# Performance work log

Hardware: AMD Instinct MI355X
Metric: run time of the kernel (lower is better)

The kernel has to match this reference:

```python
import jax, jax.numpy as jnp
import numpy as np

N = 100_000      # nodes
E = 800_000      # edges per edge type
T = 3            # num_edge_types - 1 relation-specific convs
D_IN = 128
D_OUT = 128


def setup_inputs() -> dict:
    key = jax.random.key(0)
    k1, k2, k3, k4 = jax.random.split(key, 4)
    x = jax.random.normal(k1, (N, D_IN), dtype=jnp.float32)
    edges = jax.random.randint(k2, (T, 2, E), 0, N, dtype=jnp.int32)
    W = jax.random.normal(k3, (T, D_IN, D_OUT), dtype=jnp.float32) * (1.0 / np.sqrt(D_IN))
    b = jax.random.normal(k4, (T, D_OUT), dtype=jnp.float32) * 0.02
    return {"x": x, "edges": edges, "W": W, "b": b}


def _gcn_conv(x, ei, W, b):
    """PyG GCNConv: add self-loops, symmetric D^-1/2 (A+I) D^-1/2 norm, XW, +b."""
    n = x.shape[0]
    xw = x @ W                                   # [N, D_OUT]
    loop = jnp.arange(n, dtype=ei.dtype)
    src = jnp.concatenate([ei[0], loop])         # [E+N]
    dst = jnp.concatenate([ei[1], loop])         # [E+N]
    deg = jax.ops.segment_sum(jnp.ones(src.shape[0], xw.dtype), dst, num_segments=n)
    dis = jnp.where(deg > 0, jax.lax.rsqrt(jnp.maximum(deg, 1e-12)), 0.0)
    norm = dis[src] * dis[dst]                   # [E+N]
    msg = xw[src] * norm[:, None]                # gather-transform: [E+N, D_OUT]
    out = jax.ops.segment_sum(msg, dst, num_segments=n)  # scatter-add back to nodes
    return out + b


def reference(x, edges, W, b):
    # Sum of per-edge-type GCN convolutions into a shared output buffer.
    out = jnp.zeros((x.shape[0], W.shape[-1]), dtype=x.dtype)
    for i in range(edges.shape[0]):              # small fixed relation loop
        out = out + _gcn_conv(x, edges[i], W[i], b[i])
    return out
```

## Files before the change

### kernel.cpp

```cpp
#include <hip/hip_runtime.h>

#define NN 100000
#define EE 800000
#define TT 3
#define D  128
#define NB 391
#define CAPB 7168
#define CHUNK 8192
#define LSTRIDE 392
#define ENC 32767.0f

typedef unsigned short bf16_t;

typedef __bf16 bf16x8_t __attribute__((ext_vector_type(8)));
typedef float  f32x4_t  __attribute__((ext_vector_type(4)));

union ABFrag { bf16x8_t v; uint4 q; };

__device__ __forceinline__ bf16_t f2bf(float f) {
    unsigned u = __float_as_uint(f);
    u += 0x7fff + ((u >> 16) & 1);
    return (bf16_t)(u >> 16);
}
__device__ __forceinline__ float bf_lo(unsigned p) { return __uint_as_float(p << 16); }
__device__ __forceinline__ float bf_hi(unsigned p) { return __uint_as_float(p & 0xFFFF0000u); }

__global__ void quant_kernel(const float* __restrict__ x, bf16_t* __restrict__ xq) {
    int i = (blockIdx.x * 256 + threadIdx.x) * 4;
    if (i >= NN * D) return;
    float4 f = *(const float4*)(x + i);
    uint2 p;
    p.x = (unsigned)f2bf(f.x) | ((unsigned)f2bf(f.y) << 16);
    p.y = (unsigned)f2bf(f.z) | ((unsigned)f2bf(f.w) << 16);
    *(uint2*)(xq + i) = p;
}

__global__ void wconv_kernel(const float* __restrict__ W, bf16_t* __restrict__ WT) {
    int t = blockIdx.y, n = blockIdx.x, k = threadIdx.x;
    WT[((size_t)t * D + n) * D + k] = f2bf(W[((size_t)t * D + k) * D + n]);
}

__global__ __launch_bounds__(512, 4) void bin_kernel(const int* __restrict__ edges,
                                                     int* __restrict__ bcnt,
                                                     unsigned* __restrict__ bin) {
    __shared__ int hist[NB];
    __shared__ int lbase[NB];
    __shared__ int gbase[NB];
    __shared__ int scn[512];
    __shared__ unsigned srec[CHUNK];
    __shared__ unsigned stgt[CHUNK];
    int tid = threadIdx.x;
    int t = blockIdx.y;
    int f0 = blockIdx.x * CHUNK;
    const int* sb = edges + (size_t)t * 2 * EE;
    const int* db = sb + EE;

    for (int i = tid; i < NB; i += 512) hist[i] = 0;
    __syncthreads();

    int4 s4[4], d4[4];
    int rnk[16];
    bool have[4];
#pragma unroll
    for (int j = 0; j < 4; ++j) {
        int e = f0 + ((j * 512 + tid) << 2);
        have[j] = (e < EE);
        if (have[j]) { s4[j] = *(const int4*)(sb + e); d4[j] = *(const int4*)(db + e); }
    }
#pragma unroll
    for (int j = 0; j < 4; ++j) {
        if (have[j]) {
            rnk[j * 4 + 0] = atomicAdd(&hist[d4[j].x >> 8], 1);
            rnk[j * 4 + 1] = atomicAdd(&hist[d4[j].y >> 8], 1);
            rnk[j * 4 + 2] = atomicAdd(&hist[d4[j].z >> 8], 1);
            rnk[j * 4 + 3] = atomicAdd(&hist[d4[j].w >> 8], 1);
        }
    }
    __syncthreads();

    int hv = (tid < NB) ? hist[tid] : 0;
    scn[tid] = hv;
    __syncthreads();
    for (int off = 1; off < 512; off <<= 1) {
        int u = 0;
        if (tid >= off) u = scn[tid - off];
        __syncthreads();
        if (tid >= off) scn[tid] += u;
        __syncthreads();
    }
    if (tid < NB) {
        lbase[tid] = scn[tid] - hv;
        gbase[tid] = (hv > 0) ? atomicAdd(&bcnt[tid], hv) : 0;
    }
    __syncthreads();

#pragma unroll
    for (int j = 0; j < 4; ++j) {
        if (have[j]) {
            int ss[4] = {s4[j].x, s4[j].y, s4[j].z, s4[j].w};
            int dd[4] = {d4[j].x, d4[j].y, d4[j].z, d4[j].w};
#pragma unroll
            for (int k = 0; k < 4; ++k) {
                int bkt = dd[k] >> 8;
                int r = rnk[j * 4 + k];
                int pos = lbase[bkt] + r;
                int rel = gbase[bkt] + r;
                srec[pos] = ((unsigned)(dd[k] & 255) << 19) | ((unsigned)t << 17) | (unsigned)ss[k];
                stgt[pos] = (rel < CAPB) ? (unsigned)(bkt * CAPB + rel) : 0xFFFFFFFFu;
            }
        }
    }
    __syncthreads();

    int nval = EE - f0; if (nval > CHUNK) nval = CHUNK;
    for (int i = tid; i < nval; i += 512) {
        unsigned tg = stgt[i];
        if (tg != 0xFFFFFFFFu) bin[tg] = srec[i];
    }
}

#define MAXR 14
__global__ __launch_bounds__(512) void sort_kernel(const int* __restrict__ bcnt,
                                                   unsigned* __restrict__ bin,
                                                   float* __restrict__ dis3,
                                                   int* __restrict__ cnts3,
                                                   int* __restrict__ nodeoff) {
    __shared__ int cnt[768];
    __shared__ int tot[256];
    int tid = threadIdx.x;
    int b = blockIdx.x;
    int c = bcnt[b]; if (c > CAPB) c = CAPB;
    unsigned* reg = bin + (size_t)b * CAPB;

    for (int i = tid; i < 768; i += 512) cnt[i] = 0;
    __syncthreads();

    unsigned ur[MAXR];
    int rr[MAXR];
    bool vld[MAXR];
#pragma unroll
    for (int k = 0; k < MAXR; ++k) {
        int i = tid + k * 512;
        vld[k] = (i < c);
        unsigned u = vld[k] ? reg[i] : 0u;
        ur[k] = u;
        int bi = (int)(u >> 19) * 3 + (int)((u >> 17) & 3);
        rr[k] = vld[k] ? atomicAdd(&cnt[bi], 1) : 0;
    }
    __syncthreads();

    int d0 = 0, d1 = 0, d2 = 0;
    if (tid < 256) {
        d0 = cnt[tid * 3]; d1 = cnt[tid * 3 + 1]; d2 = cnt[tid * 3 + 2];
        tot[tid] = d0 + d1 + d2;
    }
    __syncthreads();
    for (int off = 1; off < 256; off <<= 1) {
        int v = 0;
        if (tid < 256 && tid >= off) v = tot[tid - off];
        __syncthreads();
        if (tid < 256 && tid >= off) tot[tid] += v;
        __syncthreads();
    }
    if (tid < 256) {
        int excl = tot[tid] - (d0 + d1 + d2);
        int gnode = b * 256 + tid;
        if (gnode < NN) {
            nodeoff[gnode] = b * CAPB + excl;
            cnts3[gnode]   = d0 | (d1 << 8) | (d2 << 16);
            dis3[gnode]            = rsqrtf((float)d0 + 1.f);
            dis3[NN + gnode]       = rsqrtf((float)d1 + 1.f);
            dis3[2 * NN + gnode]   = rsqrtf((float)d2 + 1.f);
        }
        cnt[tid * 3]     = excl;
        cnt[tid * 3 + 1] = excl + d0;
        cnt[tid * 3 + 2] = excl + d0 + d1;
    }
    __syncthreads();
#pragma unroll
    for (int k = 0; k < MAXR; ++k) {
        if (vld[k]) {
            unsigned u = ur[k];
            int bi = (int)(u >> 19) * 3 + (int)((u >> 17) & 3);
            reg[cnt[bi] + rr[k]] = u & 0x7FFFFu;
        }
    }
}

__global__ __launch_bounds__(512) void weightize_kernel(const int* __restrict__ bcnt,
                                                        const float* __restrict__ dis3,
                                                        unsigned* __restrict__ bin) {
    int b = blockIdx.x;
    int c = bcnt[b]; if (c > CAPB) c = CAPB;
    unsigned* reg = bin + (size_t)b * CAPB;
    for (int i = threadIdx.x; i < c; i += 512) {
        unsigned u = reg[i];
        unsigned src = u & 0x1FFFFu;
        unsigned t = (u >> 17) & 3u;
        float w = dis3[t * NN + src];
        reg[i] = ((unsigned)(w * ENC + 0.5f) << 17) | src;
    }
}


#define ISSUE(UX, SA, UW, J0)                                                      \
    {                                                                              \
        const int _j0 = (J0);                                                      \
        _Pragma("unroll")                                                          \
        for (int k = 0; k < 8; ++k) {                                              \
            SA[k] = __builtin_amdgcn_readlane((int)(UW), _j0 + k);                 \
            int sxk = SA[k] & 0x1FFFF;                                             \
            UX[k] = *(const unsigned*)(xq + (size_t)sxk * D + (lane << 1));        \
        }                                                                          \
    }

#define CONSUME(UX, SA, J0, B1, B2, A00, A01, A10, A11, A20, A21)                  \
    {                                                                              \
        const int _j0 = (J0);                                                      \
        _Pragma("unroll")                                                          \
        for (int k = 0; k < 8; ++k) {                                              \
            int idxk = _j0 + k;                                                    \
            float wk = (float)(((unsigned)SA[k]) >> 17);                           \
            unsigned u = UX[k];                                                    \
            float xl = bf_lo(u), xh = bf_hi(u);                                    \
            if (idxk < B1)      { A00 += wk * xl; A01 += wk * xh; }                \
            else if (idxk < B2) { A10 += wk * xl; A11 += wk * xh; }                \
            else                { A20 += wk * xl; A21 += wk * xh; }                \
        }                                                                          \
    }

__global__ __launch_bounds__(512, 8) void fused_kernel(const bf16_t* __restrict__ xq,
                                                       const float* __restrict__ dis3,
                                                       const int* __restrict__ cnts3,
                                                       const int* __restrict__ nodeoff,
                                                       const unsigned* __restrict__ recs,
                                                       const bf16_t* __restrict__ WT,
                                                       const float* __restrict__ bias,
                                                       float* __restrict__ out) {
    __shared__ __attribute__((aligned(16))) ushort ylds[16 * LSTRIDE];
    int tid  = threadIdx.x;
    int lane = tid & 63;
    int wave = tid >> 6;
    int n0 = blockIdx.x * 16;
    int nA = n0 + wave * 2;
    int nB = nA + 1;

    unsigned suA = *(const unsigned*)(xq + (size_t)nA * D + (lane << 1));
    unsigned suB = *(const unsigned*)(xq + (size_t)nB * D + (lane << 1));
    float dnA0 = dis3[nA], dnA1 = dis3[NN + nA], dnA2 = dis3[2 * NN + nA];
    float dnB0 = dis3[nB], dnB1 = dis3[NN + nB], dnB2 = dis3[2 * NN + nB];
    int pkA = cnts3[nA], pkB = cnts3[nB];
    int s0A = nodeoff[nA], s0B = nodeoff[nB];

    int dA0 = pkA & 255, dA1 = (pkA >> 8) & 255, dA2 = (pkA >> 16) & 255;
    int dB0 = pkB & 255, dB1 = (pkB >> 8) & 255, dB2 = (pkB >> 16) & 255;

    int b1A = __builtin_amdgcn_readfirstlane(dA0);
    int b2A = __builtin_amdgcn_readfirstlane(dA0 + dA1);
    int cTA = dA0 + dA1 + dA2; if (cTA > 64) cTA = 64;
    int cSA = __builtin_amdgcn_readfirstlane(cTA);
    int b1B = __builtin_amdgcn_readfirstlane(dB0);
    int b2B = __builtin_amdgcn_readfirstlane(dB0 + dB1);
    int cTB = dB0 + dB1 + dB2; if (cTB > 64) cTB = 64;
    int cSB = __builtin_amdgcn_readfirstlane(cTB);

    unsigned uwA = recs[s0A + lane]; if (lane >= cSA) uwA = 0u;
    unsigned uwB = recs[s0B + lane]; if (lane >= cSB) uwB = 0u;

    float xsA0 = bf_lo(suA), xsA1 = bf_hi(suA);
    float xsB0 = bf_lo(suB), xsB1 = bf_hi(suB);

    float aA00 = dnA0 * ENC * xsA0, aA01 = dnA0 * ENC * xsA1;
    float aA10 = dnA1 * ENC * xsA0, aA11 = dnA1 * ENC * xsA1;
    float aA20 = dnA2 * ENC * xsA0, aA21 = dnA2 * ENC * xsA1;
    float aB00 = dnB0 * ENC * xsB0, aB01 = dnB0 * ENC * xsB1;
    float aB10 = dnB1 * ENC * xsB0, aB11 = dnB1 * ENC * xsB1;
    float aB20 = dnB2 * ENC * xsB0, aB21 = dnB2 * ENC * xsB1;

    unsigned uxA[8], uxB[8];
    int sA[8], sB[8];

    int nbA = (cSA + 7) >> 3;
    int nbB = (cSB + 7) >> 3;
    if (nbA > 0) ISSUE(uxA, sA, uwA, 0)
    if (nbB > 0) ISSUE(uxB, sB, uwB, 0)
    int nbmax = nbA > nbB ? nbA : nbB;
    for (int blk = 0; blk < nbmax; ++blk) {
        if (blk < nbA) {
            CONSUME(uxA, sA, blk * 8, b1A, b2A, aA00, aA01, aA10, aA11, aA20, aA21)
            if (blk + 1 < nbA) ISSUE(uxA, sA, uwA, (blk + 1) * 8)
        }
        if (blk < nbB) {
            CONSUME(uxB, sB, blk * 8, b1B, b2B, aB00, aB01, aB10, aB11, aB20, aB21)
            if (blk + 1 < nbB) ISSUE(uxB, sB, uwB, (blk + 1) * 8)
        }
    }

    {
        float fA0 = dnA0 * (1.0f / ENC), fA1 = dnA1 * (1.0f / ENC), fA2 = dnA2 * (1.0f / ENC);
        float fB0 = dnB0 * (1.0f / ENC), fB1 = dnB1 * (1.0f / ENC), fB2 = dnB2 * (1.0f / ENC);
        ushort* ywA = ylds + (wave * 2) * LSTRIDE + (lane << 1);
        ushort* ywB = ywA + LSTRIDE;
        *(unsigned*)(ywA)         = (unsigned)f2bf(aA00 * fA0) | ((unsigned)f2bf(aA01 * fA0) << 16);
        *(unsigned*)(ywA + D)     = (unsigned)f2bf(aA10 * fA1) | ((unsigned)f2bf(aA11 * fA1) << 16);
        *(unsigned*)(ywA + 2 * D) = (unsigned)f2bf(aA20 * fA2) | ((unsigned)f2bf(aA21 * fA2) << 16);
        *(unsigned*)(ywB)         = (unsigned)f2bf(aB00 * fB0) | ((unsigned)f2bf(aB01 * fB0) << 16);
        *(unsigned*)(ywB + D)     = (unsigned)f2bf(aB10 * fB1) | ((unsigned)f2bf(aB11 * fB1) << 16);
        *(unsigned*)(ywB + 2 * D) = (unsigned)f2bf(aB20 * fB2) | ((unsigned)f2bf(aB21 * fB2) << 16);
    }
    __syncthreads();

    {
        int quad = lane >> 4;
        int lid  = lane & 15;
        int col  = wave * 16 + lid;
        f32x4_t acc = {0.f, 0.f, 0.f, 0.f};
        const ushort* yr = ylds + lid * LSTRIDE;
#pragma unroll
        for (int t = 0; t < TT; ++t) {
            const bf16_t* wn = WT + ((size_t)t * D + col) * D;
#pragma unroll
            for (int s = 0; s < 4; ++s) {
                ABFrag av, bv;
                av.q = *(const uint4*)(yr + t * D + s * 32 + quad * 8);
                bv.q = *(const uint4*)(wn + s * 32 + quad * 8);
                acc = __builtin_amdgcn_mfma_f32_16x16x32_bf16(av.v, bv.v, acc, 0, 0, 0);
            }
        }
        float bc = bias[col] + bias[D + col] + bias[2 * D + col];
#pragma unroll
        for (int r = 0; r < 4; ++r)
            out[(size_t)(n0 + quad * 4 + r) * D + col] = acc[r] + bc;
    }
}

extern "C" void kernel_launch(void* const* d_in, const int* in_sizes, int n_in,
                              void* d_out, int out_size, void* d_ws, size_t ws_size,
                              hipStream_t stream) {
    const float* x     = (const float*)d_in[0];
    const int*   edges = (const int*)d_in[1];
    const float* W     = (const float*)d_in[2];
    const float* b     = (const float*)d_in[3];
    float*       out   = (float*)d_out;

    char* w = (char*)d_ws;
    bf16_t*   xq      = (bf16_t*)w;
    unsigned* bin     = (unsigned*)(w + (size_t)NN * D * 2);
    float*    dis3    = (float*)((char*)bin + (size_t)NB * CAPB * 4);
    int*      cnts3   = (int*)((char*)dis3 + (size_t)3 * NN * 4);
    int*      nodeoff = cnts3 + NN;
    bf16_t*   WT      = (bf16_t*)(nodeoff + NN);
    int*      bcnt    = (int*)((char*)WT + (size_t)TT * D * D * 2);

    hipMemsetAsync(bcnt, 0, (size_t)NB * sizeof(int), stream);

    quant_kernel<<<(NN * D / 4 + 255) / 256, 256, 0, stream>>>(x, xq);
    {
        dim3 g(D, TT);
        wconv_kernel<<<g, D, 0, stream>>>(W, WT);
    }

    {
        dim3 g((EE + CHUNK - 1) / CHUNK, TT);
        bin_kernel<<<g, 512, 0, stream>>>(edges, bcnt, bin);
    }

    sort_kernel<<<NB, 512, 0, stream>>>(bcnt, bin, dis3, cnts3, nodeoff);

    weightize_kernel<<<NB, 512, 0, stream>>>(bcnt, dis3, bin);

    fused_kernel<<<NN / 16, 512, 0, stream>>>(xq, dis3, cnts3, nodeoff, bin, WT, b, out);
}
```

Baseline: 304.5 us.

## Make fused kernel persistent over several node groups with prefetch of next metadata

Each block of the fused gather+MFMA kernel now handles several 16-node groups in a loop, with the grid shrunk to match. The next group's degree counts, offsets, self features and edge records are prefetched while the current group is processed. Per-node normalization is recomputed with rsqrt from the packed degree counts instead of being loaded from dis3. The aim is to hide load latency and cut launch/block overhead, at the cost of fewer resident blocks and an extra barrier per iteration.

```diff
diff --git a/kernel.cpp b/kernel.cpp
--- a/kernel.cpp
+++ b/kernel.cpp
@@ -9,6 +9,7 @@
 #define CHUNK 8192
 #define LSTRIDE 392
 #define ENC 32767.0f
+#define NITER 5
 
 typedef unsigned short bf16_t;
 
@@ -210,7 +211,7 @@
         for (int k = 0; k < 8; ++k) {                                              \
             SA[k] = __builtin_amdgcn_readlane((int)(UW), _j0 + k);                 \
             int sxk = SA[k] & 0x1FFFF;                                             \
-            UX[k] = *(const unsigned*)(xq + (size_t)sxk * D + (lane << 1));        \
+            UX[k] = *(const unsigned*)(xq + (size_t)sxk * D + lane2);              \
         }                                                                          \
     }
 
@@ -230,7 +231,6 @@
     }
 
 __global__ __launch_bounds__(512, 8) void fused_kernel(const bf16_t* __restrict__ xq,
-                                                       const float* __restrict__ dis3,
                                                        const int* __restrict__ cnts3,
                                                        const int* __restrict__ nodeoff,
                                                        const unsigned* __restrict__ recs,
@@ -241,96 +241,130 @@
     int tid  = threadIdx.x;
     int lane = tid & 63;
     int wave = tid >> 6;
-    int n0 = blockIdx.x * 16;
-    int nA = n0 + wave * 2;
-    int nB = nA + 1;
-
-    unsigned suA = *(const unsigned*)(xq + (size_t)nA * D + (lane << 1));
-    unsigned suB = *(const unsigned*)(xq + (size_t)nB * D + (lane << 1));
-    float dnA0 = dis3[nA], dnA1 = dis3[NN + nA], dnA2 = dis3[2 * NN + nA];
-    float dnB0 = dis3[nB], dnB1 = dis3[NN + nB], dnB2 = dis3[2 * NN + nB];
-    int pkA = cnts3[nA], pkB = cnts3[nB];
-    int s0A = nodeoff[nA], s0B = nodeoff[nB];
-
-    int dA0 = pkA & 255, dA1 = (pkA >> 8) & 255, dA2 = (pkA >> 16) & 255;
-    int dB0 = pkB & 255, dB1 = (pkB >> 8) & 255, dB2 = (pkB >> 16) & 255;
-
-    int b1A = __builtin_amdgcn_readfirstlane(dA0);
-    int b2A = __builtin_amdgcn_readfirstlane(dA0 + dA1);
-    int cTA = dA0 + dA1 + dA2; if (cTA > 64) cTA = 64;
-    int cSA = __builtin_amdgcn_readfirstlane(cTA);
-    int b1B = __builtin_amdgcn_readfirstlane(dB0);
-    int b2B = __builtin_amdgcn_readfirstlane(dB0 + dB1);
-    int cTB = dB0 + dB1 + dB2; if (cTB > 64) cTB = 64;
-    int cSB = __builtin_amdgcn_readfirstlane(cTB);
-
-    unsigned uwA = recs[s0A + lane]; if (lane >= cSA) uwA = 0u;
-    unsigned uwB = recs[s0B + lane]; if (lane >= cSB) uwB = 0u;
-
-    float xsA0 = bf_lo(suA), xsA1 = bf_hi(suA);
-    float xsB0 = bf_lo(suB), xsB1 = bf_hi(suB);
-
-    float aA00 = dnA0 * ENC * xsA0, aA01 = dnA0 * ENC * xsA1;
-    float aA10 = dnA1 * ENC * xsA0, aA11 = dnA1 * ENC * xsA1;
-    float aA20 = dnA2 * ENC * xsA0, aA21 = dnA2 * ENC * xsA1;
-    float aB00 = dnB0 * ENC * xsB0, aB01 = dnB0 * ENC * xsB1;
-    float aB10 = dnB1 * ENC * xsB0, aB11 = dnB1 * ENC * xsB1;
-    float aB20 = dnB2 * ENC * xsB0, aB21 = dnB2 * ENC * xsB1;
-
-    unsigned uxA[8], uxB[8];
-    int sA[8], sB[8];
-
-    int nbA = (cSA + 7) >> 3;
-    int nbB = (cSB + 7) >> 3;
-    if (nbA > 0) ISSUE(uxA, sA, uwA, 0)
-    if (nbB > 0) ISSUE(uxB, sB, uwB, 0)
-    int nbmax = nbA > nbB ? nbA : nbB;
-    for (int blk = 0; blk < nbmax; ++blk) {
-        if (blk < nbA) {
-            CONSUME(uxA, sA, blk * 8, b1A, b2A, aA00, aA01, aA10, aA11, aA20, aA21)
-            if (blk + 1 < nbA) ISSUE(uxA, sA, uwA, (blk + 1) * 8)
-        }
-        if (blk < nbB) {
-            CONSUME(uxB, sB, blk * 8, b1B, b2B, aB00, aB01, aB10, aB11, aB20, aB21)
-            if (blk + 1 < nbB) ISSUE(uxB, sB, uwB, (blk + 1) * 8)
-        }
-    }
-
-    {
-        float fA0 = dnA0 * (1.0f / ENC), fA1 = dnA1 * (1.0f / ENC), fA2 = dnA2 * (1.0f / ENC);
-        float fB0 = dnB0 * (1.0f / ENC), fB1 = dnB1 * (1.0f / ENC), fB2 = dnB2 * (1.0f / ENC);
-        ushort* ywA = ylds + (wave * 2) * LSTRIDE + (lane << 1);
-        ushort* ywB = ywA + LSTRIDE;
-        *(unsigned*)(ywA)         = (unsigned)f2bf(aA00 * fA0) | ((unsigned)f2bf(aA01 * fA0) << 16);
-        *(unsigned*)(ywA + D)     = (unsigned)f2bf(aA10 * fA1) | ((unsigned)f2bf(aA11 * fA1) << 16);
-        *(unsigned*)(ywA + 2 * D) = (unsigned)f2bf(aA20 * fA2) | ((unsigned)f2bf(aA21 * fA2) << 16);
-        *(unsigned*)(ywB)         = (unsigned)f2bf(aB00 * fB0) | ((unsigned)f2bf(aB01 * fB0) << 16);
-        *(unsigned*)(ywB + D)     = (unsigned)f2bf(aB10 * fB1) | ((unsigned)f2bf(aB11 * fB1) << 16);
-        *(unsigned*)(ywB + 2 * D) = (unsigned)f2bf(aB20 * fB2) | ((unsigned)f2bf(aB21 * fB2) << 16);
-    }
-    __syncthreads();
-
-    {
-        int quad = lane >> 4;
-        int lid  = lane & 15;
-        int col  = wave * 16 + lid;
-        f32x4_t acc = {0.f, 0.f, 0.f, 0.f};
-        const ushort* yr = ylds + lid * LSTRIDE;
-#pragma unroll
-        for (int t = 0; t < TT; ++t) {
-            const bf16_t* wn = WT + ((size_t)t * D + col) * D;
-#pragma unroll
-            for (int s = 0; s < 4; ++s) {
-                ABFrag av, bv;
-                av.q = *(const uint4*)(yr + t * D + s * 32 + quad * 8);
-                bv.q = *(const uint4*)(wn + s * 32 + quad * 8);
-                acc = __builtin_amdgcn_mfma_f32_16x16x32_bf16(av.v, bv.v, acc, 0, 0, 0);
+    int lane2 = lane << 1;
+    int grp0 = blockIdx.x * NITER;
+
+    int nA = grp0 * 16 + wave * 2;
+    int pkA = cnts3[nA],    pkB = cnts3[nA + 1];
+    int s0A = nodeoff[nA],  s0B = nodeoff[nA + 1];
+    unsigned suA = *(const unsigned*)(xq + (size_t)nA * D + lane2);
+    unsigned suB = *(const unsigned*)(xq + (size_t)(nA + 1) * D + lane2);
+    unsigned uwA = recs[s0A + lane];
+    unsigned uwB = recs[s0B + lane];
+
+    for (int g = 0; g < NITER; ++g) {
+        int n0 = (grp0 + g) * 16;
+
+        int pkA2 = 0, pkB2 = 0, s0A2 = 0, s0B2 = 0;
+        unsigned suA2 = 0, suB2 = 0;
+        if (g + 1 < NITER) {
+            int m = n0 + 16 + wave * 2;
+            pkA2 = cnts3[m];    pkB2 = cnts3[m + 1];
+            s0A2 = nodeoff[m];  s0B2 = nodeoff[m + 1];
+            suA2 = *(const unsigned*)(xq + (size_t)m * D + lane2);
+            suB2 = *(const unsigned*)(xq + (size_t)(m + 1) * D + lane2);
+        }
+
+        int dA0 = pkA & 255, dA1 = (pkA >> 8) & 255, dA2 = (pkA >> 16) & 255;
+        int dB0 = pkB & 255, dB1 = (pkB >> 8) & 255, dB2 = (pkB >> 16) & 255;
+        float dnA0 = rsqrtf((float)dA0 + 1.f), dnA1 = rsqrtf((float)dA1 + 1.f),
+              dnA2 = rsqrtf((float)dA2 + 1.f);
+        float dnB0 = rsqrtf((float)dB0 + 1.f), dnB1 = rsqrtf((float)dB1 + 1.f),
+              dnB2 = rsqrtf((float)dB2 + 1.f);
+        int b1A = __builtin_amdgcn_readfirstlane(dA0);
+        int b2A = __builtin_amdgcn_readfirstlane(dA0 + dA1);
+        int cTA = dA0 + dA1 + dA2; if (cTA > 64) cTA = 64;
+        int cSA = __builtin_amdgcn_readfirstlane(cTA);
+        int b1B = __builtin_amdgcn_readfirstlane(dB0);
+        int b2B = __builtin_amdgcn_readfirstlane(dB0 + dB1);
+        int cTB = dB0 + dB1 + dB2; if (cTB > 64) cTB = 64;
+        int cSB = __builtin_amdgcn_readfirstlane(cTB);
+
+        unsigned uwAz = (lane < cSA) ? uwA : 0u;
+        unsigned uwBz = (lane < cSB) ? uwB : 0u;
+
+        float xsA0 = bf_lo(suA), xsA1 = bf_hi(suA);
+        float xsB0 = bf_lo(suB), xsB1 = bf_hi(suB);
+
+        float aA00 = dnA0 * ENC * xsA0, aA01 = dnA0 * ENC * xsA1;
+        float aA10 = dnA1 * ENC * xsA0, aA11 = dnA1 * ENC * xsA1;
+        float aA20 = dnA2 * ENC * xsA0, aA21 = dnA2 * ENC * xsA1;
+        float aB00 = dnB0 * ENC * xsB0, aB01 = dnB0 * ENC * xsB1;
+        float aB10 = dnB1 * ENC * xsB0, aB11 = dnB1 * ENC * xsB1;
+        float aB20 = dnB2 * ENC * xsB0, aB21 = dnB2 * ENC * xsB1;
+
+        unsigned uxA[8], uxB[8];
+        int sA[8], sB[8];
+
+        int nbA = (cSA + 7) >> 3;
+        int nbB = (cSB + 7) >> 3;
+        if (nbA > 0) ISSUE(uxA, sA, uwAz, 0)
+        if (nbB > 0) ISSUE(uxB, sB, uwBz, 0)
+        int nbmax = nbA > nbB ? nbA : nbB;
+        for (int blk = 0; blk < nbmax; ++blk) {
+            if (blk < nbA) {
+                CONSUME(uxA, sA, blk * 8, b1A, b2A, aA00, aA01, aA10, aA11, aA20, aA21)
+                if (blk + 1 < nbA) ISSUE(uxA, sA, uwAz, (blk + 1) * 8)
             }
-        }
-        float bc = bias[col] + bias[D + col] + bias[2 * D + col];
-#pragma unroll
-        for (int r = 0; r < 4; ++r)
-            out[(size_t)(n0 + quad * 4 + r) * D + col] = acc[r] + bc;
+            if (blk < nbB) {
+                CONSUME(uxB, sB, blk * 8, b1B, b2B, aB00, aB01, aB10, aB11, aB20, aB21)
+                if (blk + 1 < nbB) ISSUE(uxB, sB, uwBz, (blk + 1) * 8)
+            }
+        }
+
+        unsigned uwA2 = 0, uwB2 = 0;
+        if (g + 1 < NITER) {
+            uwA2 = recs[s0A2 + lane];
+            uwB2 = recs[s0B2 + lane];
+        }
+
+        {
+            float fA0 = dnA0 * (1.0f / ENC), fA1 = dnA1 * (1.0f / ENC), fA2 = dnA2 * (1.0f / ENC);
+            float fB0 = dnB0 * (1.0f / ENC), fB1 = dnB1 * (1.0f / ENC), fB2 = dnB2 * (1.0f / ENC);
+            ushort* ywA = ylds + (wave * 2) * LSTRIDE + lane2;
+            ushort* ywB = ywA + LSTRIDE;
+            *(unsigned*)(ywA)         = (unsigned)f2bf(aA00 * fA0) | ((unsigned)f2bf(aA01 * fA0) << 16);
+            *(unsigned*)(ywA + D)     = (unsigned)f2bf(aA10 * fA1) | ((unsigned)f2bf(aA11 * fA1) << 16);
+            *(unsigned*)(ywA + 2 * D) = (unsigned)f2bf(aA20 * fA2) | ((unsigned)f2bf(aA21 * fA2) << 16);
+            *(unsigned*)(ywB)         = (unsigned)f2bf(aB00 * fB0) | ((unsigned)f2bf(aB01 * fB0) << 16);
+            *(unsigned*)(ywB + D)     = (unsigned)f2bf(aB10 * fB1) | ((unsigned)f2bf(aB11 * fB1) << 16);
+            *(unsigned*)(ywB + 2 * D) = (unsigned)f2bf(aB20 * fB2) | ((unsigned)f2bf(aB21 * fB2) << 16);
+        }
+
+        __builtin_amdgcn_sched_barrier(0);
+        asm volatile("s_waitcnt lgkmcnt(0)" ::: "memory");
+        __builtin_amdgcn_s_barrier();
+        __builtin_amdgcn_sched_barrier(0);
+
+        {
+            int quad = lane >> 4;
+            int lid  = lane & 15;
+            int col  = wave * 16 + lid;
+            f32x4_t acc = {0.f, 0.f, 0.f, 0.f};
+            const ushort* yr = ylds + lid * LSTRIDE;
+#pragma unroll
+            for (int t = 0; t < TT; ++t) {
+                const bf16_t* wn = WT + ((size_t)t * D + col) * D;
+#pragma unroll
+                for (int s = 0; s < 4; ++s) {
+                    ABFrag av, bv;
+                    av.q = *(const uint4*)(yr + t * D + s * 32 + quad * 8);
+                    bv.q = *(const uint4*)(wn + s * 32 + quad * 8);
+                    acc = __builtin_amdgcn_mfma_f32_16x16x32_bf16(av.v, bv.v, acc, 0, 0, 0);
+                }
+            }
+            float bc = bias[col] + bias[D + col] + bias[2 * D + col];
+#pragma unroll
+            for (int r = 0; r < 4; ++r)
+                out[(size_t)(n0 + quad * 4 + r) * D + col] = acc[r] + bc;
+        }
+
+        __builtin_amdgcn_sched_barrier(0);
+        __builtin_amdgcn_s_barrier();
+        __builtin_amdgcn_sched_barrier(0);
+
+        pkA = pkA2; pkB = pkB2; s0A = s0A2; s0B = s0B2;
+        suA = suA2; suB = suB2; uwA = uwA2; uwB = uwB2;
     }
 }
 
@@ -369,5 +403,5 @@
 
     weightize_kernel<<<NB, 512, 0, stream>>>(bcnt, dis3, bin);
 
-    fused_kernel<<<NN / 16, 512, 0, stream>>>(xq, dis3, cnts3, nodeoff, bin, WT, b, out);
-}
+    fused_kernel<<<NN / 16 / NITER, 512, 0, stream>>>(xq, cnts3, nodeoff, bin, WT, b, out);
+}
```

After: 349.3 us. 14.7% more time.

## Fold weightize pass into fused kernel and drop bin staging target array

Applied to the files above, without the earlier changes.

Removes the separate weightize kernel. The fused kernel now looks up each edge's normalization weight from dis3 itself and recomputes destination rsqrt from the packed degree counts. The bin kernel drops the per-record target array in shared memory and finds each record's bucket with a binary search over lbase, halving LDS so occupancy can be raised to 8 blocks. The trade is one fewer launch and one fewer pass over the bins, paid for with extra per-edge gathers in the fused kernel and a search loop in the bin scatter.

```diff
diff --git a/kernel.cpp b/kernel.cpp
--- a/kernel.cpp
+++ b/kernel.cpp
@@ -40,7 +40,7 @@
     WT[((size_t)t * D + n) * D + k] = f2bf(W[((size_t)t * D + k) * D + n]);
 }
 
-__global__ __launch_bounds__(512, 4) void bin_kernel(const int* __restrict__ edges,
+__global__ __launch_bounds__(512, 8) void bin_kernel(const int* __restrict__ edges,
                                                      int* __restrict__ bcnt,
                                                      unsigned* __restrict__ bin) {
     __shared__ int hist[NB];
@@ -48,7 +48,6 @@
     __shared__ int gbase[NB];
     __shared__ int scn[512];
     __shared__ unsigned srec[CHUNK];
-    __shared__ unsigned stgt[CHUNK];
     int tid = threadIdx.x;
     int t = blockIdx.y;
     int f0 = blockIdx.x * CHUNK;
@@ -102,11 +101,8 @@
 #pragma unroll
             for (int k = 0; k < 4; ++k) {
                 int bkt = dd[k] >> 8;
-                int r = rnk[j * 4 + k];
-                int pos = lbase[bkt] + r;
-                int rel = gbase[bkt] + r;
+                int pos = lbase[bkt] + rnk[j * 4 + k];
                 srec[pos] = ((unsigned)(dd[k] & 255) << 19) | ((unsigned)t << 17) | (unsigned)ss[k];
-                stgt[pos] = (rel < CAPB) ? (unsigned)(bkt * CAPB + rel) : 0xFFFFFFFFu;
             }
         }
     }
@@ -114,8 +110,14 @@
 
     int nval = EE - f0; if (nval > CHUNK) nval = CHUNK;
     for (int i = tid; i < nval; i += 512) {
-        unsigned tg = stgt[i];
-        if (tg != 0xFFFFFFFFu) bin[tg] = srec[i];
+        int lo = 0;
+#pragma unroll
+        for (int step = 256; step > 0; step >>= 1) {
+            int cand = lo + step;
+            if (cand < NB && lbase[cand] <= i) lo = cand;
+        }
+        int rel = gbase[lo] + (i - lbase[lo]);
+        if (rel < CAPB) bin[(size_t)lo * CAPB + rel] = srec[i];
     }
 }
 
@@ -182,23 +184,8 @@
         if (vld[k]) {
             unsigned u = ur[k];
             int bi = (int)(u >> 19) * 3 + (int)((u >> 17) & 3);
-            reg[cnt[bi] + rr[k]] = u & 0x7FFFFu;
-        }
-    }
-}
-
-__global__ __launch_bounds__(512) void weightize_kernel(const int* __restrict__ bcnt,
-                                                        const float* __restrict__ dis3,
-                                                        unsigned* __restrict__ bin) {
-    int b = blockIdx.x;
-    int c = bcnt[b]; if (c > CAPB) c = CAPB;
-    unsigned* reg = bin + (size_t)b * CAPB;
-    for (int i = threadIdx.x; i < c; i += 512) {
-        unsigned u = reg[i];
-        unsigned src = u & 0x1FFFFu;
-        unsigned t = (u >> 17) & 3u;
-        float w = dis3[t * NN + src];
-        reg[i] = ((unsigned)(w * ENC + 0.5f) << 17) | src;
+            reg[cnt[bi] + rr[k]] = u & 0x1FFFFu;
+        }
     }
 }
 
@@ -247,13 +234,15 @@
 
     unsigned suA = *(const unsigned*)(xq + (size_t)nA * D + (lane << 1));
     unsigned suB = *(const unsigned*)(xq + (size_t)nB * D + (lane << 1));
-    float dnA0 = dis3[nA], dnA1 = dis3[NN + nA], dnA2 = dis3[2 * NN + nA];
-    float dnB0 = dis3[nB], dnB1 = dis3[NN + nB], dnB2 = dis3[2 * NN + nB];
     int pkA = cnts3[nA], pkB = cnts3[nB];
     int s0A = nodeoff[nA], s0B = nodeoff[nB];
 
     int dA0 = pkA & 255, dA1 = (pkA >> 8) & 255, dA2 = (pkA >> 16) & 255;
     int dB0 = pkB & 255, dB1 = (pkB >> 8) & 255, dB2 = (pkB >> 16) & 255;
+    float dnA0 = rsqrtf((float)dA0 + 1.f), dnA1 = rsqrtf((float)dA1 + 1.f),
+          dnA2 = rsqrtf((float)dA2 + 1.f);
+    float dnB0 = rsqrtf((float)dB0 + 1.f), dnB1 = rsqrtf((float)dB1 + 1.f),
+          dnB2 = rsqrtf((float)dB2 + 1.f);
 
     int b1A = __builtin_amdgcn_readfirstlane(dA0);
     int b2A = __builtin_amdgcn_readfirstlane(dA0 + dA1);
@@ -264,8 +253,16 @@
     int cTB = dB0 + dB1 + dB2; if (cTB > 64) cTB = 64;
     int cSB = __builtin_amdgcn_readfirstlane(cTB);
 
-    unsigned uwA = recs[s0A + lane]; if (lane >= cSA) uwA = 0u;
-    unsigned uwB = recs[s0B + lane]; if (lane >= cSB) uwB = 0u;
+    unsigned urA = recs[s0A + lane];
+    unsigned urB = recs[s0B + lane];
+    int tlA = (lane < b1A) ? 0 : (lane < b2A) ? 1 : 2;
+    int tlB = (lane < b1B) ? 0 : (lane < b2B) ? 1 : 2;
+    int vsA = (int)(urA & 0x1FFFFu); if (vsA >= NN) vsA = 0;
+    int vsB = (int)(urB & 0x1FFFFu); if (vsB >= NN) vsB = 0;
+    float wsA = (lane < cSA) ? dis3[tlA * NN + vsA] : 0.0f;
+    float wsB = (lane < cSB) ? dis3[tlB * NN + vsB] : 0.0f;
+    unsigned uwA = ((unsigned)(wsA * ENC + 0.5f) << 17) | (unsigned)vsA;
+    unsigned uwB = ((unsigned)(wsB * ENC + 0.5f) << 17) | (unsigned)vsB;
 
     float xsA0 = bf_lo(suA), xsA1 = bf_hi(suA);
     float xsB0 = bf_lo(suB), xsB1 = bf_hi(suB);
@@ -367,7 +364,5 @@
 
     sort_kernel<<<NB, 512, 0, stream>>>(bcnt, bin, dis3, cnts3, nodeoff);
 
-    weightize_kernel<<<NB, 512, 0, stream>>>(bcnt, dis3, bin);
-
     fused_kernel<<<NN / 16, 512, 0, stream>>>(xq, dis3, cnts3, nodeoff, bin, WT, b, out);
 }
```

Measured after the change: 309.3 us. Within noise of the previous version (+1.6%).
